# Kernel optimization log

Hardware: AMD Instinct MI355X
Metric: run time of the kernel (lower is better)

Reference implementation:

```python
import jax, jax.numpy as jnp
import numpy as np

N_USER = 8192
N_PRODUCT = 8192
E = 128
D = 64
K = 32
M = 4


def _make_nbrs(m, n, k, n_other, salt):
    # distinct neighbor indices per (metapath, node): step = n_other // k guarantees
    # the k offsets are distinct modulo n_other (matches set-like ragged lists)
    i = np.arange(m)[:, None, None]
    j = np.arange(n)[None, :, None]
    t = np.arange(k)[None, None, :]
    idx = (j * 7 + i * 131 + salt * 17 + t * (n_other // k)) % n_other
    return jnp.asarray(idx, dtype=jnp.int32)


def setup_inputs() -> dict:
    key = jax.random.key(0)
    ks = jax.random.split(key, 16)
    s = 0.1
    return {
        "user": jax.random.normal(ks[0], (N_USER, E), jnp.float32),
        "product": jax.random.normal(ks[1], (N_PRODUCT, E), jnp.float32),
        "V": jax.random.normal(ks[2], (2, M, E, D), jnp.float32) * s,
        "X": jax.random.normal(ks[3], (2, M, 1, D), jnp.float32) * s,
        "W_p": jax.random.normal(ks[4], (2, M, E, D), jnp.float32) * s,
        "B_p": jax.random.normal(ks[5], (2, M, D), jnp.float32) * s,
        "W_q": jax.random.normal(ks[6], (2, M, E, D), jnp.float32) * s,
        "B_q": jax.random.normal(ks[7], (2, M, D), jnp.float32) * s,
        "Q": jax.random.normal(ks[8], (2, M, 1, D), jnp.float32) * s,
        "user_nbrs": _make_nbrs(M, N_USER, K, N_PRODUCT, 0),
        "product_nbrs": _make_nbrs(M, N_PRODUCT, K, N_USER, 1),
    }


def _phase(src, other, nbrs, v, x, w, b, wq, bq, q):
    # src: [n,E], other: [n_other,E], nbrs: [M,n,K] indices into other
    m, n, k = nbrs.shape
    n_other = other.shape[0]
    nbr_emb = other[nbrs]  # [M,n,K,E] ragged gather
    proj_src = jnp.einsum('ne,med->mnd', src, v)          # [M,n,D]
    proj_nbr = jnp.einsum('mnke,med->mnkd', nbr_emb, w)   # [M,n,K,D]
    h = jnp.tanh(proj_src[:, :, None, :] + proj_nbr + b[:, None, None, :])
    scores = jnp.einsum('mnkd,md->mnk', h, x[:, 0])       # [M,n,K]
    # Faithful to torch: non-neighbor logit is -1e-9 for metapath 0; for
    # metapath i>=1 the repeated whole-tensor softmax makes it 1/n_other.
    baseline = jnp.where(jnp.arange(m) == 0,
                         jnp.float32(-1e-9),
                         jnp.float32(1.0) / n_other)      # [M]
    mx = jnp.maximum(scores.max(-1), baseline[:, None])   # [M,n]
    e = jnp.exp(scores - mx[..., None])
    denom = e.sum(-1) + (n_other - k) * jnp.exp(baseline[:, None] - mx)
    A = e / denom[..., None]                              # softmax over full axis
    # H aggregation uses detached attention weights (A.data in torch)
    H = src[None] + jnp.einsum('mnk,mnke->mne', jax.lax.stop_gradient(A), nbr_emb)
    sem = jnp.tanh(jnp.einsum('mne,med->mnd', H, wq) + bq[:, None, :])
    beta_raw = jax.lax.stop_gradient(
        jnp.einsum('mnd,md->mn', sem, q[:, 0]).mean(-1))  # [M], detached (.data)
    beta = jax.nn.softmax(beta_raw)
    return jnp.einsum('m,mne->ne', beta, H)


def reference(user, product, V, X, W_p, B_p, W_q, B_q, Q, user_nbrs, product_nbrs):
    user_out = _phase(user, product, user_nbrs,
                      V[0], X[0], W_p[0], B_p[0], W_q[0], B_q[0], Q[0])
    # product phase attends over the UPDATED user embeddings
    product_out = _phase(product, user_out, product_nbrs,
                         V[1], X[1], W_p[1], B_p[1], W_q[1], B_q[1], Q[1])
    return (user_out, product_out)
```

## Files before the change

kernel.cpp:

```cpp
#include <hip/hip_runtime.h>
#include <hip/hip_bf16.h>

#define NN 8192
#define ED 128
#define DD 64
#define KK 32
#define MM 4

typedef __attribute__((ext_vector_type(8))) short short8;
typedef __attribute__((ext_vector_type(4))) float f32x4;

#if __has_builtin(__builtin_amdgcn_exp2f)
#define EXP2R(x) __builtin_amdgcn_exp2f(x)
#else
#define EXP2R(x) __expf((x) * 0.6931471805599453f)
#endif
#define C2LOG2E 2.8853900817779268f

__device__ __forceinline__ float ftanh_pre(float v)
{
    return fmaf(-2.0f, __builtin_amdgcn_rcpf(EXP2R(v) + 1.0f), 1.0f);
}
__device__ __forceinline__ float ftanh(float x)
{
    return ftanh_pre(x * C2LOG2E);
}

__device__ __forceinline__ unsigned short f2bf(float x)
{
    __hip_bfloat16 b = __float2bfloat16(x);
    return *reinterpret_cast<unsigned short*>(&b);
}
__device__ __forceinline__ float bflo(unsigned int u) { return __uint_as_float(u << 16); }
__device__ __forceinline__ float bfhi(unsigned int u) { return __uint_as_float(u & 0xFFFF0000u); }
__device__ __forceinline__ float readlane_f(float v, int lane)
{
    return __uint_as_float(__builtin_amdgcn_readlane(__float_as_uint(v), lane));
}

template <int CTRL>
__device__ __forceinline__ float dpp_mov_f(float x)
{
    return __int_as_float(__builtin_amdgcn_update_dpp(
        0, __float_as_int(x), CTRL, 0xF, 0xF, true));
}
template <int CTRL>
__device__ __forceinline__ float dpp_add_f(float x)
{
    return x + dpp_mov_f<CTRL>(x);
}

__global__ __launch_bounds__(256) void prep_kernel(
    const float* __restrict__ user, unsigned short* __restrict__ userB,
    const float* __restrict__ product, unsigned short* __restrict__ productB,
    const float* __restrict__ V, unsigned short* __restrict__ VT,
    const float* __restrict__ Wp, unsigned short* __restrict__ PT,
    const float* __restrict__ Wq, unsigned short* __restrict__ QT)
{
    const int y = blockIdx.y;
    if (y < 2) {
        const float* in = y ? product : user;
        unsigned short* out = y ? productB : userB;
        const int i = blockIdx.x * 256 + threadIdx.x;
        const float4 v = ((const float4*)in)[i];
        uint2 o;
        o.x = (unsigned int)f2bf(v.x) | ((unsigned int)f2bf(v.y) << 16);
        o.y = (unsigned int)f2bf(v.z) | ((unsigned int)f2bf(v.w) << 16);
        ((uint2*)out)[i] = o;
    } else {
        if (blockIdx.x >= 256) return;
        const float* in = (y == 2) ? V : (y == 3) ? Wp : Wq;
        unsigned short* out = (y == 2) ? VT : (y == 3) ? PT : QT;
        const int gid = blockIdx.x * 256 + threadIdx.x;
        const int s   = gid >> 13;
        const int rem = gid & 8191;
        const int e   = rem >> 6;
        const int d   = rem & 63;
        out[((size_t)s * DD + d) * ED + e] = f2bf(in[gid]);
    }
}

__global__ __launch_bounds__(256) void proj3_mfma(
    const unsigned short* __restrict__ emb0,
    const unsigned short* __restrict__ Wt0,
    const float* __restrict__ Bias0,
    float* __restrict__ outF0,
    const unsigned short* __restrict__ emb1,
    const unsigned short* __restrict__ Wt1,
    unsigned short* __restrict__ outB1,
    const unsigned short* __restrict__ Wt2,
    const float* __restrict__ Bias2,
    float* __restrict__ outF2)
{
    const int z    = blockIdx.z;
    const int m    = blockIdx.y;
    const int tid  = threadIdx.x;
    const int wave = tid >> 6;
    const int lane = tid & 63;
    const int nrow = lane & 15;
    const int quad = lane >> 4;
    const int r0   = blockIdx.x * 64 + wave * 16;

    const unsigned short* embB = (z == 0) ? emb0 : emb1;
    const unsigned short* WtB  = (z == 0) ? Wt0 : (z == 1) ? Wt1 : Wt2;

    const short8* A8 = (const short8*)(embB + (size_t)(r0 + nrow) * ED);
    const short8* B8 = (const short8*)(WtB + (size_t)m * DD * ED);

    f32x4 acc0 = {0.f, 0.f, 0.f, 0.f};
    f32x4 acc1 = {0.f, 0.f, 0.f, 0.f};
    f32x4 acc2 = {0.f, 0.f, 0.f, 0.f};
    f32x4 acc3 = {0.f, 0.f, 0.f, 0.f};

    #pragma unroll
    for (int kq = 0; kq < 4; ++kq) {
        const short8 a = A8[kq * 4 + quad];
        const short8 b0 = B8[(0 * 16 + nrow) * 16 + kq * 4 + quad];
        const short8 b1 = B8[(1 * 16 + nrow) * 16 + kq * 4 + quad];
        const short8 b2 = B8[(2 * 16 + nrow) * 16 + kq * 4 + quad];
        const short8 b3 = B8[(3 * 16 + nrow) * 16 + kq * 4 + quad];
        acc0 = __builtin_amdgcn_mfma_f32_16x16x32_bf16(a, b0, acc0, 0, 0, 0);
        acc1 = __builtin_amdgcn_mfma_f32_16x16x32_bf16(a, b1, acc1, 0, 0, 0);
        acc2 = __builtin_amdgcn_mfma_f32_16x16x32_bf16(a, b2, acc2, 0, 0, 0);
        acc3 = __builtin_amdgcn_mfma_f32_16x16x32_bf16(a, b3, acc3, 0, 0, 0);
    }

    f32x4 accs[4] = {acc0, acc1, acc2, acc3};
    if (z == 1) {
        #pragma unroll
        for (int t = 0; t < 4; ++t) {
            const int d = t * 16 + nrow;
            #pragma unroll
            for (int reg = 0; reg < 4; ++reg) {
                const int r = r0 + quad * 4 + reg;
                outB1[((size_t)m * NN + r) * DD + d] =
                    f2bf(EXP2R(accs[t][reg] * C2LOG2E));
            }
        }
    } else {
        const float* Bi = (z == 0) ? Bias0 : Bias2;
        float* oF       = (z == 0) ? outF0 : outF2;
        #pragma unroll
        for (int t = 0; t < 4; ++t) {
            const int d = t * 16 + nrow;
            const float bv = Bi[m * DD + d];
            #pragma unroll
            for (int reg = 0; reg < 4; ++reg) {
                const int r = r0 + quad * 4 + reg;
                oF[((size_t)m * NN + r) * DD + d] =
                    EXP2R((accs[t][reg] + bv) * C2LOG2E);
            }
        }
    }
}

__global__ __launch_bounds__(512) void attn_sem_kernel(
    const float* __restrict__ src,
    const unsigned short* __restrict__ otherB,
    const int*   __restrict__ nbrs,
    const float* __restrict__ S,
    const unsigned short* __restrict__ PnB,
    const float* __restrict__ Xv,
    unsigned short* __restrict__ HoutB,
    const unsigned short* __restrict__ WqT,
    const float* __restrict__ Bq,
    const float* __restrict__ Qv,
    float* __restrict__ bp)
{
    __shared__ __align__(16) unsigned int lh[16][68];
    __shared__ float red_sh[4];

    const int m    = blockIdx.y;
    const int tid  = threadIdx.x;
    const int w    = tid >> 6;
    const int lane = tid & 63;
    const int g    = blockIdx.x * 8 + w;
    const int j0   = g * 2;
    const int j1   = g * 2 + 1;

    const int kr = lane >> 3;
    const int d8 = lane & 7;

    const int jj = (lane < 32) ? j0 : j1;
    const int idxreg = nbrs[((size_t)m * NN + jj) * KK + (lane & 31)];

    float S0c[8], S1c[8], m2X[8];
    float sumX;
    {
        const float4 a0 = *(const float4*)(S + ((size_t)m * NN + j0) * DD + d8 * 8);
        const float4 a1 = *(const float4*)(S + ((size_t)m * NN + j0) * DD + d8 * 8 + 4);
        const float4 b0 = *(const float4*)(S + ((size_t)m * NN + j1) * DD + d8 * 8);
        const float4 b1 = *(const float4*)(S + ((size_t)m * NN + j1) * DD + d8 * 8 + 4);
        const float4 x0 = *(const float4*)(Xv + (size_t)m * DD + d8 * 8);
        const float4 x1 = *(const float4*)(Xv + (size_t)m * DD + d8 * 8 + 4);
        S0c[0]=a0.x; S0c[1]=a0.y; S0c[2]=a0.z; S0c[3]=a0.w;
        S0c[4]=a1.x; S0c[5]=a1.y; S0c[6]=a1.z; S0c[7]=a1.w;
        S1c[0]=b0.x; S1c[1]=b0.y; S1c[2]=b0.z; S1c[3]=b0.w;
        S1c[4]=b1.x; S1c[5]=b1.y; S1c[6]=b1.z; S1c[7]=b1.w;
        m2X[0]=-2.0f*x0.x; m2X[1]=-2.0f*x0.y; m2X[2]=-2.0f*x0.z; m2X[3]=-2.0f*x0.w;
        m2X[4]=-2.0f*x1.x; m2X[5]=-2.0f*x1.y; m2X[6]=-2.0f*x1.z; m2X[7]=-2.0f*x1.w;
        sumX = ((x0.x + x0.y) + (x0.z + x0.w)) + ((x1.x + x1.y) + (x1.z + x1.w));
    }
    const float2 hs0 = ((const float2*)(src + (size_t)j0 * ED))[lane];
    const float2 hs1 = ((const float2*)(src + (size_t)j1 * ED))[lane];

    int sk0[4], sk1[4];
    #pragma unroll
    for (int i = 0; i < 4; ++i) {
        const int k = i * 8 + kr;
        sk0[i] = __shfl(idxreg, k, 64);
        sk1[i] = __shfl(idxreg, 32 + k, 64);
    }
    uint4 P0[4], P1[4];
    #pragma unroll
    for (int i = 0; i < 4; ++i) {
        P0[i] = ((const uint4*)(PnB + ((size_t)m * NN + sk0[i]) * DD))[d8];
        P1[i] = ((const uint4*)(PnB + ((size_t)m * NN + sk1[i]) * DD))[d8];
    }

    float ea0[4], ea1[4];
    #pragma unroll
    for (int i = 0; i < 4; ++i) {
        const unsigned int pw0[4] = {P0[i].x, P0[i].y, P0[i].z, P0[i].w};
        const unsigned int pw1[4] = {P1[i].x, P1[i].y, P1[i].z, P1[i].w};
        float q0 = sumX, q1 = sumX;
        #pragma unroll
        for (int c = 0; c < 4; ++c) {
            const float lo0 = bflo(pw0[c]), hi0 = bfhi(pw0[c]);
            const float lo1 = bflo(pw1[c]), hi1 = bfhi(pw1[c]);
            float r;
            r = __builtin_amdgcn_rcpf(fmaf(lo0, S0c[c*2  ], 1.0f));
            q0 = fmaf(m2X[c*2  ], r, q0);
            r = __builtin_amdgcn_rcpf(fmaf(lo1, S1c[c*2  ], 1.0f));
            q1 = fmaf(m2X[c*2  ], r, q1);
            r = __builtin_amdgcn_rcpf(fmaf(hi0, S0c[c*2+1], 1.0f));
            q0 = fmaf(m2X[c*2+1], r, q0);
            r = __builtin_amdgcn_rcpf(fmaf(hi1, S1c[c*2+1], 1.0f));
            q1 = fmaf(m2X[c*2+1], r, q1);
        }
        q0 = dpp_add_f<0xB1>(q0);   q1 = dpp_add_f<0xB1>(q1);
        q0 = dpp_add_f<0x4E>(q0);   q1 = dpp_add_f<0x4E>(q1);
        q0 = dpp_add_f<0x141>(q0);  q1 = dpp_add_f<0x141>(q1);
        ea0[i] = q0;
        ea1[i] = q1;
    }

    const float baseline = (m == 0) ? -1e-9f : (1.0f / (float)NN);
    float mx0 = ea0[0], mx1 = ea1[0];
    #pragma unroll
    for (int i = 1; i < 4; ++i) { mx0 = fmaxf(mx0, ea0[i]); mx1 = fmaxf(mx1, ea1[i]); }
    mx0 = fmaxf(mx0, dpp_mov_f<0x128>(mx0));
    mx1 = fmaxf(mx1, dpp_mov_f<0x128>(mx1));
    mx0 = fmaxf(mx0, __shfl_xor(mx0, 16, 64));
    mx1 = fmaxf(mx1, __shfl_xor(mx1, 16, 64));
    mx0 = fmaxf(mx0, __shfl_xor(mx0, 32, 64));
    mx1 = fmaxf(mx1, __shfl_xor(mx1, 32, 64));
    mx0 = fmaxf(mx0, baseline);
    mx1 = fmaxf(mx1, baseline);
    float sum0 = 0.0f, sum1 = 0.0f;
    #pragma unroll
    for (int i = 0; i < 4; ++i) {
        ea0[i] = __expf(ea0[i] - mx0); sum0 += ea0[i];
        ea1[i] = __expf(ea1[i] - mx1); sum1 += ea1[i];
    }
    sum0 = dpp_add_f<0x128>(sum0);
    sum1 = dpp_add_f<0x128>(sum1);
    sum0 += __shfl_xor(sum0, 16, 64);  sum1 += __shfl_xor(sum1, 16, 64);
    sum0 += __shfl_xor(sum0, 32, 64);  sum1 += __shfl_xor(sum1, 32, 64);
    const float inv0 =
        __builtin_amdgcn_rcpf(sum0 + (float)(NN - KK) * __expf(baseline - mx0));
    const float inv1 =
        __builtin_amdgcn_rcpf(sum1 + (float)(NN - KK) * __expf(baseline - mx1));
    #pragma unroll
    for (int i = 0; i < 4; ++i) { ea0[i] *= inv0; ea1[i] *= inv1; }

    float2 ha = hs0, hb = hs1;
    unsigned int cur0[4], cur1[4], nxt0[4], nxt1[4];
    #pragma unroll
    for (int t = 0; t < 4; ++t) {
        const int ja = __builtin_amdgcn_readlane(idxreg, t);
        const int jb = __builtin_amdgcn_readlane(idxreg, 32 + t);
        cur0[t] = ((const unsigned int*)(otherB + (size_t)ja * ED))[lane];
        cur1[t] = ((const unsigned int*)(otherB + (size_t)jb * ED))[lane];
    }
    #pragma unroll
    for (int c = 0; c < 8; ++c) {
        if (c < 7) {
            #pragma unroll
            for (int t = 0; t < 4; ++t) {
                const int k2 = (c + 1) * 4 + t;
                const int ja = __builtin_amdgcn_readlane(idxreg, k2);
                const int jb = __builtin_amdgcn_readlane(idxreg, 32 + k2);
                nxt0[t] = ((const unsigned int*)(otherB + (size_t)ja * ED))[lane];
                nxt1[t] = ((const unsigned int*)(otherB + (size_t)jb * ED))[lane];
            }
        }
        #pragma unroll
        for (int t = 0; t < 4; ++t) {
            const int k  = c * 4 + t;
            const float a0 = readlane_f(ea0[k >> 3], (k & 7) * 8);
            const float a1 = readlane_f(ea1[k >> 3], (k & 7) * 8);
            ha.x = fmaf(a0, bflo(cur0[t]), ha.x);
            hb.x = fmaf(a1, bflo(cur1[t]), hb.x);
            ha.y = fmaf(a0, bfhi(cur0[t]), ha.y);
            hb.y = fmaf(a1, bfhi(cur1[t]), hb.y);
        }
        #pragma unroll
        for (int t = 0; t < 4; ++t) { cur0[t] = nxt0[t]; cur1[t] = nxt1[t]; }
    }
    const unsigned int hu0 =
        (unsigned int)f2bf(ha.x) | ((unsigned int)f2bf(ha.y) << 16);
    const unsigned int hu1 =
        (unsigned int)f2bf(hb.x) | ((unsigned int)f2bf(hb.y) << 16);
    ((unsigned int*)(HoutB + ((size_t)m * NN + j0) * ED))[lane] = hu0;
    ((unsigned int*)(HoutB + ((size_t)m * NN + j1) * ED))[lane] = hu1;

    lh[w * 2    ][lane] = hu0;
    lh[w * 2 + 1][lane] = hu1;
    __syncthreads();

    if (w < 4) {
        const int nrow = lane & 15;
        const int quad = lane >> 4;
        const short8* B8 = (const short8*)(WqT + (size_t)m * DD * ED);
        const short8* A8 = (const short8*)&lh[nrow][0];
        f32x4 acc = {0.f, 0.f, 0.f, 0.f};
        #pragma unroll
        for (int kq = 0; kq < 4; ++kq) {
            const short8 a = A8[kq * 4 + quad];
            const short8 b = B8[(w * 16 + nrow) * 16 + kq * 4 + quad];
            acc = __builtin_amdgcn_mfma_f32_16x16x32_bf16(a, b, acc, 0, 0, 0);
        }
        const int d = w * 16 + nrow;
        const float bq = Bq[m * DD + d];
        const float qv = Qv[m * DD + d];
        float part = 0.0f;
        #pragma unroll
        for (int reg = 0; reg < 4; ++reg)
            part = fmaf(ftanh(acc[reg] + bq), qv, part);
        #pragma unroll
        for (int off = 32; off; off >>= 1) part += __shfl_xor(part, off, 64);
        if (lane == 0) red_sh[w] = part;
    }
    __syncthreads();
    if (tid == 0)
        bp[m * 512 + blockIdx.x] =
            (red_sh[0] + red_sh[1]) + (red_sh[2] + red_sh[3]);
}

__global__ __launch_bounds__(256) void combine_proj(
    const unsigned short* __restrict__ HB,
    const float* __restrict__ bp,
    float* __restrict__ outp,
    unsigned short* __restrict__ outB,
    const unsigned short* __restrict__ WtE,
    unsigned short* __restrict__ EPo)
{
    __shared__ float bw_sh[4];
    const int tid = threadIdx.x;
    if (tid < 64) {
        const int m = tid >> 4, t = tid & 15;
        float s = 0.0f;
        #pragma unroll
        for (int i = 0; i < 32; ++i)
            s += bp[m * 512 + t + i * 16];
        s += __shfl_xor(s, 1, 64);
        s += __shfl_xor(s, 2, 64);
        s += __shfl_xor(s, 4, 64);
        s += __shfl_xor(s, 8, 64);
        const float v = s * (1.0f / (float)NN);
        float mx = v;
        mx = fmaxf(mx, __shfl_xor(mx, 16, 64));
        mx = fmaxf(mx, __shfl_xor(mx, 32, 64));
        const float e = expf(v - mx);
        float es = e;
        es += __shfl_xor(es, 16, 64);
        es += __shfl_xor(es, 32, 64);
        if (t == 0) bw_sh[m] = e / es;
    }
    __syncthreads();
    const float bw0 = bw_sh[0], bw1 = bw_sh[1], bw2 = bw_sh[2], bw3 = bw_sh[3];

    const int wave = tid >> 6;
    const int lane = tid & 63;
    const int nrow = lane & 15;
    const int quad = lane >> 4;
    const int r0   = blockIdx.x * 64 + wave * 16;
    const int r    = r0 + nrow;
    const size_t st = (size_t)NN * ED;

    short8 afrag[4];
    #pragma unroll
    for (int kq = 0; kq < 4; ++kq) {
        const int col = kq * 32 + quad * 8;
        const size_t off = (size_t)r * ED + col;
        const uint4 v0 = *(const uint4*)(HB + 0 * st + off);
        const uint4 v1 = *(const uint4*)(HB + 1 * st + off);
        const uint4 v2 = *(const uint4*)(HB + 2 * st + off);
        const uint4 v3 = *(const uint4*)(HB + 3 * st + off);
        const unsigned int u0[4] = {v0.x, v0.y, v0.z, v0.w};
        const unsigned int u1[4] = {v1.x, v1.y, v1.z, v1.w};
        const unsigned int u2[4] = {v2.x, v2.y, v2.z, v2.w};
        const unsigned int u3[4] = {v3.x, v3.y, v3.z, v3.w};
        float a[8];
        #pragma unroll
        for (int c = 0; c < 4; ++c) {
            a[2*c]   = fmaf(bw0, bflo(u0[c]), fmaf(bw1, bflo(u1[c]),
                       fmaf(bw2, bflo(u2[c]), bw3 * bflo(u3[c]))));
            a[2*c+1] = fmaf(bw0, bfhi(u0[c]), fmaf(bw1, bfhi(u1[c]),
                       fmaf(bw2, bfhi(u2[c]), bw3 * bfhi(u3[c]))));
        }
        float4 o1; o1.x = a[0]; o1.y = a[1]; o1.z = a[2]; o1.w = a[3];
        float4 o2; o2.x = a[4]; o2.y = a[5]; o2.z = a[6]; o2.w = a[7];
        *(float4*)(outp + off)     = o1;
        *(float4*)(outp + off + 4) = o2;
        uint4 ob;
        ob.x = (unsigned int)f2bf(a[0]) | ((unsigned int)f2bf(a[1]) << 16);
        ob.y = (unsigned int)f2bf(a[2]) | ((unsigned int)f2bf(a[3]) << 16);
        ob.z = (unsigned int)f2bf(a[4]) | ((unsigned int)f2bf(a[5]) << 16);
        ob.w = (unsigned int)f2bf(a[6]) | ((unsigned int)f2bf(a[7]) << 16);
        *(uint4*)(outB + off) = ob;
        union { uint4 u; short8 s; } pk;
        pk.u = ob;
        afrag[kq] = pk.s;
    }

    const short8* B8 = (const short8*)WtE;
    #pragma unroll
    for (int m = 0; m < MM; ++m) {
        f32x4 acc0 = {0.f, 0.f, 0.f, 0.f};
        f32x4 acc1 = {0.f, 0.f, 0.f, 0.f};
        f32x4 acc2 = {0.f, 0.f, 0.f, 0.f};
        f32x4 acc3 = {0.f, 0.f, 0.f, 0.f};
        #pragma unroll
        for (int kq = 0; kq < 4; ++kq) {
            const short8 a = afrag[kq];
            const short8 b0 = B8[((size_t)m * DD + 0 * 16 + nrow) * 16 + kq * 4 + quad];
            const short8 b1 = B8[((size_t)m * DD + 1 * 16 + nrow) * 16 + kq * 4 + quad];
            const short8 b2 = B8[((size_t)m * DD + 2 * 16 + nrow) * 16 + kq * 4 + quad];
            const short8 b3 = B8[((size_t)m * DD + 3 * 16 + nrow) * 16 + kq * 4 + quad];
            acc0 = __builtin_amdgcn_mfma_f32_16x16x32_bf16(a, b0, acc0, 0, 0, 0);
            acc1 = __builtin_amdgcn_mfma_f32_16x16x32_bf16(a, b1, acc1, 0, 0, 0);
            acc2 = __builtin_amdgcn_mfma_f32_16x16x32_bf16(a, b2, acc2, 0, 0, 0);
            acc3 = __builtin_amdgcn_mfma_f32_16x16x32_bf16(a, b3, acc3, 0, 0, 0);
        }
        f32x4 accs[4] = {acc0, acc1, acc2, acc3};
        #pragma unroll
        for (int t = 0; t < 4; ++t) {
            const int d = t * 16 + nrow;
            #pragma unroll
            for (int reg = 0; reg < 4; ++reg) {
                const int rr = r0 + quad * 4 + reg;
                EPo[((size_t)m * NN + rr) * DD + d] =
                    f2bf(EXP2R(accs[t][reg] * C2LOG2E));
            }
        }
    }
}

__global__ __launch_bounds__(256) void combine_kernel(
    const unsigned short* __restrict__ HB,
    const float* __restrict__ bp,
    float* __restrict__ outp)
{
    __shared__ float bw_sh[4];
    const int tid = threadIdx.x;
    if (tid < 64) {
        const int m = tid >> 4, t = tid & 15;
        float s = 0.0f;
        #pragma unroll
        for (int i = 0; i < 32; ++i)
            s += bp[m * 512 + t + i * 16];
        s += __shfl_xor(s, 1, 64);
        s += __shfl_xor(s, 2, 64);
        s += __shfl_xor(s, 4, 64);
        s += __shfl_xor(s, 8, 64);
        const float v = s * (1.0f / (float)NN);
        float mx = v;
        mx = fmaxf(mx, __shfl_xor(mx, 16, 64));
        mx = fmaxf(mx, __shfl_xor(mx, 32, 64));
        const float e = expf(v - mx);
        float es = e;
        es += __shfl_xor(es, 16, 64);
        es += __shfl_xor(es, 32, 64);
        if (t == 0) bw_sh[m] = e / es;
    }
    __syncthreads();

    const int i = blockIdx.x * 256 + tid;
    const size_t st = (size_t)NN * ED / 4;
    const uint2* h = (const uint2*)HB;
    float r0 = 0.f, r1 = 0.f, r2 = 0.f, r3 = 0.f;
    #pragma unroll
    for (int s = 0; s < MM; ++s) {
        const float b = bw_sh[s];
        const uint2 v = h[s * st + i];
        r0 = fmaf(b, bflo(v.x), r0);
        r1 = fmaf(b, bfhi(v.x), r1);
        r2 = fmaf(b, bflo(v.y), r2);
        r3 = fmaf(b, bfhi(v.y), r3);
    }
    float4 o; o.x = r0; o.y = r1; o.z = r2; o.w = r3;
    ((float4*)outp)[i] = o;
}

extern "C" void kernel_launch(void* const* d_in, const int* in_sizes, int n_in,
                              void* d_out, int out_size, void* d_ws, size_t ws_size,
                              hipStream_t stream)
{
    const float* user    = (const float*)d_in[0];
    const float* product = (const float*)d_in[1];
    const float* V   = (const float*)d_in[2];
    const float* X   = (const float*)d_in[3];
    const float* W_p = (const float*)d_in[4];
    const float* B_p = (const float*)d_in[5];
    const float* W_q = (const float*)d_in[6];
    const float* B_q = (const float*)d_in[7];
    const float* Q   = (const float*)d_in[8];
    const int* user_nbrs    = (const int*)d_in[9];
    const int* product_nbrs = (const int*)d_in[10];

    float* out  = (float*)d_out;
    float* out0 = out;
    float* out1 = out + (size_t)NN * ED;

    float* ws = (float*)d_ws;
    float* bp = ws;
    float* S  = bp + 2048;
    float* S2 = S + (size_t)MM * NN * DD;
    unsigned short* us = (unsigned short*)(S2 + (size_t)MM * NN * DD);
    unsigned short* PnB      = us;
    unsigned short* HB       = PnB + (size_t)MM * NN * DD;
    unsigned short* userB    = HB + (size_t)MM * NN * ED;
    unsigned short* productB = userB + (size_t)NN * ED;
    unsigned short* oB       = productB + (size_t)NN * ED;
    unsigned short* VT       = oB + (size_t)NN * ED;
    unsigned short* PT       = VT + (size_t)2 * MM * DD * ED;
    unsigned short* QT       = PT + (size_t)2 * MM * DD * ED;

    const size_t MED = (size_t)MM * ED * DD;
    const size_t MD  = (size_t)MM * DD;

    const dim3 gP(NN / 64, MM, 3);
    const dim3 gA(NN / 16, MM);
    const int cBlocks = (NN * ED / 4) / 256;

    prep_kernel<<<dim3(1024, 5), 256, 0, stream>>>(user, userB, product, productB,
                                                   V, VT, W_p, PT, W_q, QT);

    proj3_mfma<<<gP, 256, 0, stream>>>(userB, VT, B_p, S,
                                       productB, PT, PnB,
                                       VT + MED, B_p + MD, S2);

    attn_sem_kernel<<<gA, 512, 0, stream>>>(user, productB, user_nbrs,
                                            S, PnB, X, HB,
                                            QT, B_q, Q, bp);

    combine_proj<<<NN / 64, 256, 0, stream>>>(HB, bp, out0, oB,
                                              PT + MED, PnB);

    attn_sem_kernel<<<gA, 512, 0, stream>>>(product, oB, product_nbrs,
                                            S2, PnB, X + MD, HB,
                                            QT + MED, B_q + MD, Q + MD, bp);

    combine_kernel<<<cBlocks, 256, 0, stream>>>(HB, bp, out1);
}
```

Baseline: 184.9 us.

## Pack FMAs into float2 vectors, deepen gather prefetch, split combine_proj across metapaths

The attention-score and aggregation loops now use two-wide float vector FMAs so the compiler can emit packed FP32 instructions. The neighbor-embedding gather prefetch goes from double to triple buffering, keeping two chunks in flight. combine_proj gets a metapath grid dimension, so each block runs one metapath's MFMA projection instead of looping over all four. Every block recomputes the combine step and only metapath-0 blocks write the outputs, which adds redundant combine work and register pressure.

Measured after the change: 182.9 us. No clear change (-1.1%).

```diff
diff --git a/kernel.cpp b/kernel.cpp
--- a/kernel.cpp
+++ b/kernel.cpp
@@ -9,6 +9,7 @@
 
 typedef __attribute__((ext_vector_type(8))) short short8;
 typedef __attribute__((ext_vector_type(4))) float f32x4;
+typedef __attribute__((ext_vector_type(2))) float f32x2;
 
 #if __has_builtin(__builtin_amdgcn_exp2f)
 #define EXP2R(x) __builtin_amdgcn_exp2f(x)
@@ -16,6 +17,18 @@
 #define EXP2R(x) __expf((x) * 0.6931471805599453f)
 #endif
 #define C2LOG2E 2.8853900817779268f
+
+#if __has_builtin(__builtin_elementwise_fma)
+#define FMA2(a, b, c) __builtin_elementwise_fma((a), (b), (c))
+#else
+__device__ __forceinline__ f32x2 FMA2(f32x2 a, f32x2 b, f32x2 c)
+{
+    f32x2 r;
+    r.x = fmaf(a.x, b.x, c.x);
+    r.y = fmaf(a.y, b.y, c.y);
+    return r;
+}
+#endif
 
 __device__ __forceinline__ float ftanh_pre(float v)
 {
@@ -184,7 +197,7 @@
     const int jj = (lane < 32) ? j0 : j1;
     const int idxreg = nbrs[((size_t)m * NN + jj) * KK + (lane & 31)];
 
-    float S0c[8], S1c[8], m2X[8];
+    f32x2 S0v[4], S1v[4], m2Xv[4];
     float sumX;
     {
         const float4 a0 = *(const float4*)(S + ((size_t)m * NN + j0) * DD + d8 * 8);
@@ -193,12 +206,14 @@
         const float4 b1 = *(const float4*)(S + ((size_t)m * NN + j1) * DD + d8 * 8 + 4);
         const float4 x0 = *(const float4*)(Xv + (size_t)m * DD + d8 * 8);
         const float4 x1 = *(const float4*)(Xv + (size_t)m * DD + d8 * 8 + 4);
-        S0c[0]=a0.x; S0c[1]=a0.y; S0c[2]=a0.z; S0c[3]=a0.w;
-        S0c[4]=a1.x; S0c[5]=a1.y; S0c[6]=a1.z; S0c[7]=a1.w;
-        S1c[0]=b0.x; S1c[1]=b0.y; S1c[2]=b0.z; S1c[3]=b0.w;
-        S1c[4]=b1.x; S1c[5]=b1.y; S1c[6]=b1.z; S1c[7]=b1.w;
-        m2X[0]=-2.0f*x0.x; m2X[1]=-2.0f*x0.y; m2X[2]=-2.0f*x0.z; m2X[3]=-2.0f*x0.w;
-        m2X[4]=-2.0f*x1.x; m2X[5]=-2.0f*x1.y; m2X[6]=-2.0f*x1.z; m2X[7]=-2.0f*x1.w;
+        S0v[0] = (f32x2){a0.x, a0.y}; S0v[1] = (f32x2){a0.z, a0.w};
+        S0v[2] = (f32x2){a1.x, a1.y}; S0v[3] = (f32x2){a1.z, a1.w};
+        S1v[0] = (f32x2){b0.x, b0.y}; S1v[1] = (f32x2){b0.z, b0.w};
+        S1v[2] = (f32x2){b1.x, b1.y}; S1v[3] = (f32x2){b1.z, b1.w};
+        m2Xv[0] = (f32x2){-2.0f * x0.x, -2.0f * x0.y};
+        m2Xv[1] = (f32x2){-2.0f * x0.z, -2.0f * x0.w};
+        m2Xv[2] = (f32x2){-2.0f * x1.x, -2.0f * x1.y};
+        m2Xv[3] = (f32x2){-2.0f * x1.z, -2.0f * x1.w};
         sumX = ((x0.x + x0.y) + (x0.z + x0.w)) + ((x1.x + x1.y) + (x1.z + x1.w));
     }
     const float2 hs0 = ((const float2*)(src + (size_t)j0 * ED))[lane];
@@ -218,26 +233,30 @@
         P1[i] = ((const uint4*)(PnB + ((size_t)m * NN + sk1[i]) * DD))[d8];
     }
 
+    const f32x2 ones = {1.0f, 1.0f};
     float ea0[4], ea1[4];
     #pragma unroll
     for (int i = 0; i < 4; ++i) {
         const unsigned int pw0[4] = {P0[i].x, P0[i].y, P0[i].z, P0[i].w};
         const unsigned int pw1[4] = {P1[i].x, P1[i].y, P1[i].z, P1[i].w};
-        float q0 = sumX, q1 = sumX;
+        f32x2 q0v = {sumX, 0.0f};
+        f32x2 q1v = {sumX, 0.0f};
         #pragma unroll
         for (int c = 0; c < 4; ++c) {
-            const float lo0 = bflo(pw0[c]), hi0 = bfhi(pw0[c]);
-            const float lo1 = bflo(pw1[c]), hi1 = bfhi(pw1[c]);
-            float r;
-            r = __builtin_amdgcn_rcpf(fmaf(lo0, S0c[c*2  ], 1.0f));
-            q0 = fmaf(m2X[c*2  ], r, q0);
-            r = __builtin_amdgcn_rcpf(fmaf(lo1, S1c[c*2  ], 1.0f));
-            q1 = fmaf(m2X[c*2  ], r, q1);
-            r = __builtin_amdgcn_rcpf(fmaf(hi0, S0c[c*2+1], 1.0f));
-            q0 = fmaf(m2X[c*2+1], r, q0);
-            r = __builtin_amdgcn_rcpf(fmaf(hi1, S1c[c*2+1], 1.0f));
-            q1 = fmaf(m2X[c*2+1], r, q1);
-        }
+            const f32x2 p0 = {bflo(pw0[c]), bfhi(pw0[c])};
+            const f32x2 p1 = {bflo(pw1[c]), bfhi(pw1[c])};
+            const f32x2 t0 = FMA2(p0, S0v[c], ones);
+            const f32x2 t1 = FMA2(p1, S1v[c], ones);
+            f32x2 r0, r1;
+            r0.x = __builtin_amdgcn_rcpf(t0.x);
+            r0.y = __builtin_amdgcn_rcpf(t0.y);
+            r1.x = __builtin_amdgcn_rcpf(t1.x);
+            r1.y = __builtin_amdgcn_rcpf(t1.y);
+            q0v = FMA2(m2Xv[c], r0, q0v);
+            q1v = FMA2(m2Xv[c], r1, q1v);
+        }
+        float q0 = q0v.x + q0v.y;
+        float q1 = q1v.x + q1v.y;
         q0 = dpp_add_f<0xB1>(q0);   q1 = dpp_add_f<0xB1>(q1);
         q0 = dpp_add_f<0x4E>(q0);   q1 = dpp_add_f<0x4E>(q1);
         q0 = dpp_add_f<0x141>(q0);  q1 = dpp_add_f<0x141>(q1);
@@ -274,25 +293,32 @@
     #pragma unroll
     for (int i = 0; i < 4; ++i) { ea0[i] *= inv0; ea1[i] *= inv1; }
 
-    float2 ha = hs0, hb = hs1;
-    unsigned int cur0[4], cur1[4], nxt0[4], nxt1[4];
-    #pragma unroll
-    for (int t = 0; t < 4; ++t) {
-        const int ja = __builtin_amdgcn_readlane(idxreg, t);
-        const int jb = __builtin_amdgcn_readlane(idxreg, 32 + t);
-        cur0[t] = ((const unsigned int*)(otherB + (size_t)ja * ED))[lane];
-        cur1[t] = ((const unsigned int*)(otherB + (size_t)jb * ED))[lane];
+    f32x2 ha = {hs0.x, hs0.y};
+    f32x2 hb = {hs1.x, hs1.y};
+    unsigned int b0[3][4], b1[3][4];
+    #pragma unroll
+    for (int p = 0; p < 2; ++p) {
+        #pragma unroll
+        for (int t = 0; t < 4; ++t) {
+            const int k2 = p * 4 + t;
+            const int ja = __builtin_amdgcn_readlane(idxreg, k2);
+            const int jb = __builtin_amdgcn_readlane(idxreg, 32 + k2);
+            b0[p][t] = ((const unsigned int*)(otherB + (size_t)ja * ED))[lane];
+            b1[p][t] = ((const unsigned int*)(otherB + (size_t)jb * ED))[lane];
+        }
     }
     #pragma unroll
     for (int c = 0; c < 8; ++c) {
-        if (c < 7) {
+        const int slot  = c % 3;
+        const int nslot = (c + 2) % 3;
+        if (c < 6) {
             #pragma unroll
             for (int t = 0; t < 4; ++t) {
-                const int k2 = (c + 1) * 4 + t;
+                const int k2 = (c + 2) * 4 + t;
                 const int ja = __builtin_amdgcn_readlane(idxreg, k2);
                 const int jb = __builtin_amdgcn_readlane(idxreg, 32 + k2);
-                nxt0[t] = ((const unsigned int*)(otherB + (size_t)ja * ED))[lane];
-                nxt1[t] = ((const unsigned int*)(otherB + (size_t)jb * ED))[lane];
+                b0[nslot][t] = ((const unsigned int*)(otherB + (size_t)ja * ED))[lane];
+                b1[nslot][t] = ((const unsigned int*)(otherB + (size_t)jb * ED))[lane];
             }
         }
         #pragma unroll
@@ -300,13 +326,13 @@
             const int k  = c * 4 + t;
             const float a0 = readlane_f(ea0[k >> 3], (k & 7) * 8);
             const float a1 = readlane_f(ea1[k >> 3], (k & 7) * 8);
-            ha.x = fmaf(a0, bflo(cur0[t]), ha.x);
-            hb.x = fmaf(a1, bflo(cur1[t]), hb.x);
-            ha.y = fmaf(a0, bfhi(cur0[t]), ha.y);
-            hb.y = fmaf(a1, bfhi(cur1[t]), hb.y);
-        }
-        #pragma unroll
-        for (int t = 0; t < 4; ++t) { cur0[t] = nxt0[t]; cur1[t] = nxt1[t]; }
+            const f32x2 av0 = {a0, a0};
+            const f32x2 av1 = {a1, a1};
+            const f32x2 e0 = {bflo(b0[slot][t]), bfhi(b0[slot][t])};
+            const f32x2 e1 = {bflo(b1[slot][t]), bfhi(b1[slot][t])};
+            ha = FMA2(av0, e0, ha);
+            hb = FMA2(av1, e1, hb);
+        }
     }
     const unsigned int hu0 =
         (unsigned int)f2bf(ha.x) | ((unsigned int)f2bf(ha.y) << 16);
@@ -381,6 +407,8 @@
     __syncthreads();
     const float bw0 = bw_sh[0], bw1 = bw_sh[1], bw2 = bw_sh[2], bw3 = bw_sh[3];
 
+    const int mB   = blockIdx.y;
+    const bool writer = (mB == 0);
     const int wave = tid >> 6;
     const int lane = tid & 63;
     const int nrow = lane & 15;
@@ -410,50 +438,49 @@
             a[2*c+1] = fmaf(bw0, bfhi(u0[c]), fmaf(bw1, bfhi(u1[c]),
                        fmaf(bw2, bfhi(u2[c]), bw3 * bfhi(u3[c]))));
         }
-        float4 o1; o1.x = a[0]; o1.y = a[1]; o1.z = a[2]; o1.w = a[3];
-        float4 o2; o2.x = a[4]; o2.y = a[5]; o2.z = a[6]; o2.w = a[7];
-        *(float4*)(outp + off)     = o1;
-        *(float4*)(outp + off + 4) = o2;
         uint4 ob;
         ob.x = (unsigned int)f2bf(a[0]) | ((unsigned int)f2bf(a[1]) << 16);
         ob.y = (unsigned int)f2bf(a[2]) | ((unsigned int)f2bf(a[3]) << 16);
         ob.z = (unsigned int)f2bf(a[4]) | ((unsigned int)f2bf(a[5]) << 16);
         ob.w = (unsigned int)f2bf(a[6]) | ((unsigned int)f2bf(a[7]) << 16);
-        *(uint4*)(outB + off) = ob;
+        if (writer) {
+            float4 o1; o1.x = a[0]; o1.y = a[1]; o1.z = a[2]; o1.w = a[3];
+            float4 o2; o2.x = a[4]; o2.y = a[5]; o2.z = a[6]; o2.w = a[7];
+            *(float4*)(outp + off)     = o1;
+            *(float4*)(outp + off + 4) = o2;
+            *(uint4*)(outB + off) = ob;
+        }
         union { uint4 u; short8 s; } pk;
         pk.u = ob;
         afrag[kq] = pk.s;
     }
 
-    const short8* B8 = (const short8*)WtE;
-    #pragma unroll
-    for (int m = 0; m < MM; ++m) {
-        f32x4 acc0 = {0.f, 0.f, 0.f, 0.f};
-        f32x4 acc1 = {0.f, 0.f, 0.f, 0.f};
-        f32x4 acc2 = {0.f, 0.f, 0.f, 0.f};
-        f32x4 acc3 = {0.f, 0.f, 0.f, 0.f};
-        #pragma unroll
-        for (int kq = 0; kq < 4; ++kq) {
-            const short8 a = afrag[kq];
-            const short8 b0 = B8[((size_t)m * DD + 0 * 16 + nrow) * 16 + kq * 4 + quad];
-            const short8 b1 = B8[((size_t)m * DD + 1 * 16 + nrow) * 16 + kq * 4 + quad];
-            const short8 b2 = B8[((size_t)m * DD + 2 * 16 + nrow) * 16 + kq * 4 + quad];
-            const short8 b3 = B8[((size_t)m * DD + 3 * 16 + nrow) * 16 + kq * 4 + quad];
-            acc0 = __builtin_amdgcn_mfma_f32_16x16x32_bf16(a, b0, acc0, 0, 0, 0);
-            acc1 = __builtin_amdgcn_mfma_f32_16x16x32_bf16(a, b1, acc1, 0, 0, 0);
-            acc2 = __builtin_amdgcn_mfma_f32_16x16x32_bf16(a, b2, acc2, 0, 0, 0);
-            acc3 = __builtin_amdgcn_mfma_f32_16x16x32_bf16(a, b3, acc3, 0, 0, 0);
-        }
-        f32x4 accs[4] = {acc0, acc1, acc2, acc3};
-        #pragma unroll
-        for (int t = 0; t < 4; ++t) {
-            const int d = t * 16 + nrow;
-            #pragma unroll
-            for (int reg = 0; reg < 4; ++reg) {
-                const int rr = r0 + quad * 4 + reg;
-                EPo[((size_t)m * NN + rr) * DD + d] =
-                    f2bf(EXP2R(accs[t][reg] * C2LOG2E));
-            }
+    const short8* B8 = (const short8*)(WtE + (size_t)mB * DD * ED);
+    f32x4 acc0 = {0.f, 0.f, 0.f, 0.f};
+    f32x4 acc1 = {0.f, 0.f, 0.f, 0.f};
+    f32x4 acc2 = {0.f, 0.f, 0.f, 0.f};
+    f32x4 acc3 = {0.f, 0.f, 0.f, 0.f};
+    #pragma unroll
+    for (int kq = 0; kq < 4; ++kq) {
+        const short8 a = afrag[kq];
+        const short8 w0 = B8[(0 * 16 + nrow) * 16 + kq * 4 + quad];
+        const short8 w1 = B8[(1 * 16 + nrow) * 16 + kq * 4 + quad];
+        const short8 w2 = B8[(2 * 16 + nrow) * 16 + kq * 4 + quad];
+        const short8 w3 = B8[(3 * 16 + nrow) * 16 + kq * 4 + quad];
+        acc0 = __builtin_amdgcn_mfma_f32_16x16x32_bf16(a, w0, acc0, 0, 0, 0);
+        acc1 = __builtin_amdgcn_mfma_f32_16x16x32_bf16(a, w1, acc1, 0, 0, 0);
+        acc2 = __builtin_amdgcn_mfma_f32_16x16x32_bf16(a, w2, acc2, 0, 0, 0);
+        acc3 = __builtin_amdgcn_mfma_f32_16x16x32_bf16(a, w3, acc3, 0, 0, 0);
+    }
+    f32x4 accs[4] = {acc0, acc1, acc2, acc3};
+    #pragma unroll
+    for (int t = 0; t < 4; ++t) {
+        const int d = t * 16 + nrow;
+        #pragma unroll
+        for (int reg = 0; reg < 4; ++reg) {
+            const int rr = r0 + quad * 4 + reg;
+            EPo[((size_t)mB * NN + rr) * DD + d] =
+                f2bf(EXP2R(accs[t][reg] * C2LOG2E));
         }
     }
 }
@@ -543,6 +570,7 @@
 
     const dim3 gP(NN / 64, MM, 3);
     const dim3 gA(NN / 16, MM);
+    const dim3 gC(NN / 64, MM);
     const int cBlocks = (NN * ED / 4) / 256;
 
     prep_kernel<<<dim3(1024, 5), 256, 0, stream>>>(user, userB, product, productB,
@@ -556,8 +584,8 @@
                                             S, PnB, X, HB,
                                             QT, B_q, Q, bp);
 
-    combine_proj<<<NN / 64, 256, 0, stream>>>(HB, bp, out0, oB,
-                                              PT + MED, PnB);
+    combine_proj<<<gC, 256, 0, stream>>>(HB, bp, out0, oB,
+                                         PT + MED, PnB);
 
     attn_sem_kernel<<<gA, 512, 0, stream>>>(product, oB, product_nbrs,
                                             S2, PnB, X + MD, HB,
```
